# Performance work log

Hardware: AMD Instinct MI355X
Metric: run time of the kernel (lower is better)

Reference implementation:

```python
import jax, jax.numpy as jnp
import numpy as np

# slax LIF defaults
INIT_TAU = 2.0
BETA = jax.nn.sigmoid(INIT_TAU)  # membrane leak factor
VTH = 1.0                        # spike threshold
SLOPE = 25.0                     # fast-sigmoid surrogate slope

@jax.custom_vjp
def spike_fn(v):
    # heaviside forward, fast-sigmoid surrogate backward
    return (v >= 0.0).astype(v.dtype)

def _spike_fwd(v):
    return spike_fn(v), v

def _spike_bwd(v, g):
    return (g / (SLOPE * jnp.abs(v) + 1.0) ** 2,)

spike_fn.defvjp(_spike_fwd, _spike_bwd)


def setup_inputs() -> dict:
    key = jax.random.key(0)
    k1, k2 = jax.random.split(key, 2)
    B, T, F = 256, 2000, 128
    x = jax.random.normal(k1, (B, T, F), jnp.float32)
    # Dense(1) params (lecun_normal-ish init, zero bias)
    W = jax.random.normal(k2, (F, 1), jnp.float32) / jnp.sqrt(F)
    b = jnp.zeros((1,), jnp.float32)
    return {"x": x, "W": W, "b": b}


def reference(x, W, b):
    # Dense(1): [B,T,F] -> [B,T,1]
    cur = x @ W + b
    B = cur.shape[0]
    v0 = jnp.zeros((B, 1), cur.dtype)

    def step(v, c):
        v = BETA * v + c                  # leaky integrate
        s = spike_fn(v - VTH)             # threshold
        v = v - s * VTH                   # subtraction reset
        return v, s

    vT, spikes = jax.lax.scan(step, v0, jnp.swapaxes(cur, 0, 1))  # scan over time
    spikes = jnp.swapaxes(spikes, 0, 1)   # [B,T,1]
    return spikes, vT                     # (spike train, final Vmem)
```

## Files before the change

kernel.cpp:

```cpp
#include <hip/hip_runtime.h>

#define B_DIM   256
#define T_STEPS 2000
#define F_DIM   128
#define TILE    256
#define NT      8

__global__ __launch_bounds__(1024) void lif_fused2(
    const float* __restrict__ x, const float* __restrict__ W,
    const float* __restrict__ bias, float* __restrict__ out, int B) {
  const float BETA = 0.8807970779778823f;

  __shared__ __align__(16) float buf[2][TILE];

  const int tid  = threadIdx.x;
  const int lane = tid & 63;
  const int wave = tid >> 6;
  const int sub  = lane & 15;
  const int grp  = lane >> 4;
  const int b    = blockIdx.x;

  const float4 wlo = ((const float4*)W)[sub];
  const float4 whi = ((const float4*)W)[sub + 16];
  const float  bs  = bias[0];
  const float* xb  = x + (size_t)b * T_STEPS * F_DIM;
  float* outb = out + (size_t)b * T_STEPS;

  float4 xl[4], xh[4];
  float  v = 0.0f;

  auto tileLen = [&](int c) {
    const int t0 = c * TILE;
    return (T_STEPS - t0 < TILE) ? (T_STEPS - t0) : TILE;
  };

  auto loadRegs = [&](int c) {
    const int t0 = c * TILE, len = tileLen(c);
#pragma unroll
    for (int q = 0; q < 4; ++q) {
      const int tl = wave * 16 + q * 4;
      if (tl < len) {
        const float4* row = (const float4*)(xb + (size_t)(t0 + tl + grp) * F_DIM);
        xl[q] = row[sub];
        xh[q] = row[sub + 16];
      }
    }
  };

  auto reduceTo = [&](float* dst, int c) {
    const int len = tileLen(c);
#pragma unroll
    for (int q = 0; q < 4; ++q) {
      const int tl = wave * 16 + q * 4;
      if (tl < len) {
        float pl = xl[q].x * wlo.x;
        pl = fmaf(xl[q].y, wlo.y, pl);
        pl = fmaf(xl[q].z, wlo.z, pl);
        pl = fmaf(xl[q].w, wlo.w, pl);
        float ph = xh[q].x * whi.x;
        ph = fmaf(xh[q].y, whi.y, ph);
        ph = fmaf(xh[q].z, whi.z, ph);
        ph = fmaf(xh[q].w, whi.w, ph);
        float s = pl + ph;
        s += __shfl_xor(s, 8, 64);
        s += __shfl_xor(s, 4, 64);
        s += __shfl_xor(s, 2, 64);
        s += __shfl_xor(s, 1, 64);
        if (sub == 0) dst[tl + grp] = s + bs;
      }
    }
  };

  loadRegs(0);
  reduceTo(buf[0], 0);
  __syncthreads();

  for (int c = 0; c < NT; ++c) {
    if (c + 1 < NT) loadRegs(c + 1);

    if (wave == 0) {
      const float* cb  = buf[c & 1];
      const int    t0  = c * TILE;
      const int    len = tileLen(c);
      const int    ng  = len >> 3;
      float sreg = 0.0f;

      auto step = [&](float cvv, int tloc) {
        const float vp   = __fadd_rn(__fmul_rn(BETA, v), cvv);
        const bool  fire = (vp >= 1.0f);
        v = fire ? __fsub_rn(vp, 1.0f) : vp;
        const float s = fire ? 1.0f : 0.0f;
        if ((tloc & 63) == lane) sreg = s;
      };

      float4 A0 = *(const float4*)&cb[0];
      float4 A1 = *(const float4*)&cb[4];
      for (int gg = 0; gg < ng; gg += 2) {
        float4 Bq0 = *(const float4*)&cb[(gg + 1) * 8];
        float4 Bq1 = *(const float4*)&cb[(gg + 1) * 8 + 4];
        step(A0.x, gg * 8 + 0); step(A0.y, gg * 8 + 1);
        step(A0.z, gg * 8 + 2); step(A0.w, gg * 8 + 3);
        step(A1.x, gg * 8 + 4); step(A1.y, gg * 8 + 5);
        step(A1.z, gg * 8 + 6); step(A1.w, gg * 8 + 7);
        if (gg + 2 < ng) {
          A0 = *(const float4*)&cb[(gg + 2) * 8];
          A1 = *(const float4*)&cb[(gg + 2) * 8 + 4];
        }
        const int tb = (gg + 1) * 8;
        step(Bq0.x, tb + 0); step(Bq0.y, tb + 1);
        step(Bq0.z, tb + 2); step(Bq0.w, tb + 3);
        step(Bq1.x, tb + 4); step(Bq1.y, tb + 5);
        step(Bq1.z, tb + 6); step(Bq1.w, tb + 7);
        if (((gg + 1) & 7) == 7) {
          const int tend = tb + 7;
          outb[t0 + (tend - 63) + lane] = sreg;
        }
      }
      const int rem = len & 63;
      if (rem && lane < rem)
        outb[t0 + (len & ~63) + lane] = sreg;
    }

    if (c + 1 < NT) reduceTo(buf[(c + 1) & 1], c + 1);
    __syncthreads();
  }

  if (tid == 0) out[(size_t)B_DIM * T_STEPS + b] = v;
}

extern "C" void kernel_launch(void* const* d_in, const int* in_sizes, int n_in,
                              void* d_out, int out_size, void* d_ws, size_t ws_size,
                              hipStream_t stream) {
  const float* x    = (const float*)d_in[0];
  const float* W    = (const float*)d_in[1];
  const float* bias = (const float*)d_in[2];
  float* out = (float*)d_out;
  const int B = in_sizes[0] / (T_STEPS * F_DIM);
  lif_fused2<<<dim3(B), dim3(1024), 0, stream>>>(x, W, bias, out, B);
}
```

Before: 363.7 us.

## Replace barrier-synchronized double buffer with flag-based ring buffer producer/consumer

Swaps the per-tile __syncthreads double buffer for an 8-slot shared-memory ring. Producer waves fill slots, signal through per-slot atomic counters and wait only on a 'done' flag, while wave 0 consumes the scan two tiles behind. This is meant to decouple the serial scan from the loads and dot-product reductions so the loads can run ahead without block-wide barriers. The cost is spin-wait polling with s_sleep, atomics, and the risk of deadlock or scheduling contention when wave 0 is both producer and consumer.

```diff
diff --git a/kernel.cpp b/kernel.cpp
--- a/kernel.cpp
+++ b/kernel.cpp
@@ -5,13 +5,17 @@
 #define F_DIM   128
 #define TILE    256
 #define NT      8
+#define RING    8
+#define DSCAN   2
 
-__global__ __launch_bounds__(1024) void lif_fused2(
+__global__ __launch_bounds__(1024) void lif_fused3(
     const float* __restrict__ x, const float* __restrict__ W,
     const float* __restrict__ bias, float* __restrict__ out, int B) {
   const float BETA = 0.8807970779778823f;
 
-  __shared__ __align__(16) float buf[2][TILE];
+  __shared__ __align__(16) float ring[RING][TILE];
+  __shared__ int arr[RING];
+  __shared__ int done;
 
   const int tid  = threadIdx.x;
   const int lane = tid & 63;
@@ -20,22 +24,32 @@
   const int grp  = lane >> 4;
   const int b    = blockIdx.x;
 
+  if (tid < RING) arr[tid] = 0;
+  if (tid == 0)   done = -1;
+  __syncthreads();
+
   const float4 wlo = ((const float4*)W)[sub];
   const float4 whi = ((const float4*)W)[sub + 16];
   const float  bs  = bias[0];
   const float* xb  = x + (size_t)b * T_STEPS * F_DIM;
   float* outb = out + (size_t)b * T_STEPS;
 
-  float4 xl[4], xh[4];
-  float  v = 0.0f;
+  float v = 0.0f;
 
   auto tileLen = [&](int c) {
     const int t0 = c * TILE;
     return (T_STEPS - t0 < TILE) ? (T_STEPS - t0) : TILE;
   };
 
-  auto loadRegs = [&](int c) {
-    const int t0 = c * TILE, len = tileLen(c);
+  auto produce = [&](int k) {
+    const int s   = k & (RING - 1);
+    const int t0  = k * TILE;
+    const int len = tileLen(k);
+    while (__hip_atomic_load(&done, __ATOMIC_ACQUIRE,
+                             __HIP_MEMORY_SCOPE_WORKGROUP) < k - RING)
+      __builtin_amdgcn_s_sleep(1);
+
+    float4 xl[4], xh[4];
 #pragma unroll
     for (int q = 0; q < 4; ++q) {
       const int tl = wave * 16 + q * 4;
@@ -45,10 +59,7 @@
         xh[q] = row[sub + 16];
       }
     }
-  };
-
-  auto reduceTo = [&](float* dst, int c) {
-    const int len = tileLen(c);
+    float* dst = ring[s];
 #pragma unroll
     for (int q = 0; q < 4; ++q) {
       const int tl = wave * 16 + q * 4;
@@ -61,69 +72,83 @@
         ph = fmaf(xh[q].y, whi.y, ph);
         ph = fmaf(xh[q].z, whi.z, ph);
         ph = fmaf(xh[q].w, whi.w, ph);
-        float s = pl + ph;
-        s += __shfl_xor(s, 8, 64);
-        s += __shfl_xor(s, 4, 64);
-        s += __shfl_xor(s, 2, 64);
-        s += __shfl_xor(s, 1, 64);
-        if (sub == 0) dst[tl + grp] = s + bs;
+        float sum = pl + ph;
+        sum += __shfl_xor(sum, 8, 64);
+        sum += __shfl_xor(sum, 4, 64);
+        sum += __shfl_xor(sum, 2, 64);
+        sum += __shfl_xor(sum, 1, 64);
+        if (sub == 0) dst[tl + grp] = sum + bs;
       }
+    }
+    __threadfence_block();
+    if (lane == 0) atomicAdd(&arr[s], 1);
+  };
+
+  auto consume = [&](int k) {
+    const int s   = k & (RING - 1);
+    const int t0  = k * TILE;
+    const int len = tileLen(k);
+    while (__hip_atomic_load(&arr[s], __ATOMIC_ACQUIRE,
+                             __HIP_MEMORY_SCOPE_WORKGROUP) != 16)
+      __builtin_amdgcn_s_sleep(1);
+
+    const float* cb = ring[s];
+    const int    ng = len >> 3;
+    float sreg = 0.0f;
+
+    auto step = [&](float cvv, int tloc) {
+      const float vp   = __fadd_rn(__fmul_rn(BETA, v), cvv);
+      const bool  fire = (vp >= 1.0f);
+      v = fire ? __fsub_rn(vp, 1.0f) : vp;
+      const float sv = fire ? 1.0f : 0.0f;
+      if ((tloc & 63) == lane) sreg = sv;
+    };
+
+    float4 A0 = *(const float4*)&cb[0];
+    float4 A1 = *(const float4*)&cb[4];
+    for (int gg = 0; gg < ng; gg += 2) {
+      float4 Bq0 = *(const float4*)&cb[(gg + 1) * 8];
+      float4 Bq1 = *(const float4*)&cb[(gg + 1) * 8 + 4];
+      step(A0.x, gg * 8 + 0); step(A0.y, gg * 8 + 1);
+      step(A0.z, gg * 8 + 2); step(A0.w, gg * 8 + 3);
+      step(A1.x, gg * 8 + 4); step(A1.y, gg * 8 + 5);
+      step(A1.z, gg * 8 + 6); step(A1.w, gg * 8 + 7);
+      if (gg + 2 < ng) {
+        A0 = *(const float4*)&cb[(gg + 2) * 8];
+        A1 = *(const float4*)&cb[(gg + 2) * 8 + 4];
+      }
+      const int tb = (gg + 1) * 8;
+      step(Bq0.x, tb + 0); step(Bq0.y, tb + 1);
+      step(Bq0.z, tb + 2); step(Bq0.w, tb + 3);
+      step(Bq1.x, tb + 4); step(Bq1.y, tb + 5);
+      step(Bq1.z, tb + 6); step(Bq1.w, tb + 7);
+      if (((gg + 1) & 7) == 7) {
+        const int tend = tb + 7;
+        outb[t0 + (tend - 63) + lane] = sreg;
+      }
+    }
+    const int rem = len & 63;
+    if (rem && lane < rem)
+      outb[t0 + (len & ~63) + lane] = sreg;
+
+    __threadfence_block();
+    if (lane == 0) {
+      __hip_atomic_store(&arr[s], 0, __ATOMIC_RELAXED,
+                         __HIP_MEMORY_SCOPE_WORKGROUP);
+      __threadfence_block();
+      __hip_atomic_store(&done, k, __ATOMIC_RELEASE,
+                         __HIP_MEMORY_SCOPE_WORKGROUP);
     }
   };
 
-  loadRegs(0);
-  reduceTo(buf[0], 0);
+  for (int k = 0; k < NT; ++k) {
+    produce(k);
+    if (wave == 0 && k >= DSCAN) consume(k - DSCAN);
+  }
+  if (wave == 0) {
+    for (int k = NT - DSCAN; k < NT; ++k) consume(k);
+  }
   __syncthreads();
-
-  for (int c = 0; c < NT; ++c) {
-    if (c + 1 < NT) loadRegs(c + 1);
-
-    if (wave == 0) {
-      const float* cb  = buf[c & 1];
-      const int    t0  = c * TILE;
-      const int    len = tileLen(c);
-      const int    ng  = len >> 3;
-      float sreg = 0.0f;
-
-      auto step = [&](float cvv, int tloc) {
-        const float vp   = __fadd_rn(__fmul_rn(BETA, v), cvv);
-        const bool  fire = (vp >= 1.0f);
-        v = fire ? __fsub_rn(vp, 1.0f) : vp;
-        const float s = fire ? 1.0f : 0.0f;
-        if ((tloc & 63) == lane) sreg = s;
-      };
-
-      float4 A0 = *(const float4*)&cb[0];
-      float4 A1 = *(const float4*)&cb[4];
-      for (int gg = 0; gg < ng; gg += 2) {
-        float4 Bq0 = *(const float4*)&cb[(gg + 1) * 8];
-        float4 Bq1 = *(const float4*)&cb[(gg + 1) * 8 + 4];
-        step(A0.x, gg * 8 + 0); step(A0.y, gg * 8 + 1);
-        step(A0.z, gg * 8 + 2); step(A0.w, gg * 8 + 3);
-        step(A1.x, gg * 8 + 4); step(A1.y, gg * 8 + 5);
-        step(A1.z, gg * 8 + 6); step(A1.w, gg * 8 + 7);
-        if (gg + 2 < ng) {
-          A0 = *(const float4*)&cb[(gg + 2) * 8];
-          A1 = *(const float4*)&cb[(gg + 2) * 8 + 4];
-        }
-        const int tb = (gg + 1) * 8;
-        step(Bq0.x, tb + 0); step(Bq0.y, tb + 1);
-        step(Bq0.z, tb + 2); step(Bq0.w, tb + 3);
-        step(Bq1.x, tb + 4); step(Bq1.y, tb + 5);
-        step(Bq1.z, tb + 6); step(Bq1.w, tb + 7);
-        if (((gg + 1) & 7) == 7) {
-          const int tend = tb + 7;
-          outb[t0 + (tend - 63) + lane] = sreg;
-        }
-      }
-      const int rem = len & 63;
-      if (rem && lane < rem)
-        outb[t0 + (len & ~63) + lane] = sreg;
-    }
-
-    if (c + 1 < NT) reduceTo(buf[(c + 1) & 1], c + 1);
-    __syncthreads();
-  }
 
   if (tid == 0) out[(size_t)B_DIM * T_STEPS + b] = v;
 }
@@ -136,5 +161,5 @@
   const float* bias = (const float*)d_in[2];
   float* out = (float*)d_out;
   const int B = in_sizes[0] / (T_STEPS * F_DIM);
-  lif_fused2<<<dim3(B), dim3(1024), 0, stream>>>(x, W, bias, out, B);
+  lif_fused3<<<dim3(B), dim3(1024), 0, stream>>>(x, W, bias, out, B);
 }
```

Result: slower. 398.6 us (+9.6%).
